# Performance work log

Hardware: AMD Instinct MI355X
Metric: run time of the kernel (lower is better)

Reference implementation:

```python
import jax, jax.numpy as jnp
import numpy as np
import math

INC, OUTC, N, STRIDE = 128, 256, 9, 1
B, H, W = 8, 64, 64
EPS = 1e-5


def setup_inputs() -> dict:
    key = jax.random.key(0)
    k0, k1, k2, k3 = jax.random.split(key, 4)
    x = jax.random.normal(k0, (B, INC, H, W), jnp.float32)
    # p_conv: 3x3 conv inc -> 2N (torch inits weight=0; use small random so offsets are nontrivial)
    pw = jax.random.normal(k1, (2 * N, INC, 3, 3), jnp.float32) * 0.01
    pb = jax.random.normal(k2, (2 * N,), jnp.float32) * 0.01
    # final 1x1 conv inc -> outc (bias=None in the module), BN affine params
    cw = jax.random.normal(k3, (OUTC, INC, 1, 1), jnp.float32) * (1.0 / math.sqrt(INC))
    gamma = jnp.ones((OUTC,), jnp.float32)
    beta = jnp.zeros((OUTC,), jnp.float32)
    return dict(x=x, pw=pw, pb=pb, cw=cw, gamma=gamma, beta=beta)


def _akconv(x, pw, pb, cw, gamma, beta):
    b, c, Hx, Wx = x.shape
    # offset = p_conv(x): 3x3 conv, padding 1, stride STRIDE -> (b, 2N, h, w)
    offset = jax.lax.conv_general_dilated(
        x, pw, window_strides=(STRIDE, STRIDE), padding=((1, 1), (1, 1)),
        dimension_numbers=("NCHW", "OIHW", "NCHW")) + pb[None, :, None, None]
    h, w = offset.shape[2], offset.shape[3]

    # p_n: N points on unit circle (x=cos, y=sin), concat -> (2N,)
    angles = jnp.linspace(0.0, 2.0 * math.pi, N + 1)[:-1]
    p_n = jnp.concatenate([jnp.cos(angles), jnp.sin(angles)])  # (2N,)

    # p_0: base grid positions, (2N, h, w)
    gx = jnp.broadcast_to((jnp.arange(h, dtype=jnp.float32) * STRIDE)[:, None], (h, w))
    gy = jnp.broadcast_to((jnp.arange(w, dtype=jnp.float32) * STRIDE)[None, :], (h, w))
    p0 = jnp.concatenate([jnp.broadcast_to(gx[None], (N, h, w)),
                          jnp.broadcast_to(gy[None], (N, h, w))], axis=0)

    p = (offset + p_n[None, :, None, None] + p0[None]).transpose(0, 2, 3, 1)  # (b,h,w,2N)
    px, py = p[..., :N], p[..., N:]

    fx = jnp.floor(jax.lax.stop_gradient(px))  # q is detached in the original
    fy = jnp.floor(jax.lax.stop_gradient(py))
    q_ltx = jnp.clip(fx, 0, Hx - 1)
    q_lty = jnp.clip(fy, 0, Wx - 1)
    q_rbx = jnp.clip(fx + 1.0, 0, Hx - 1)
    q_rby = jnp.clip(fy + 1.0, 0, Wx - 1)
    pxc = jnp.clip(px, 0, Hx - 1)
    pyc = jnp.clip(py, 0, Wx - 1)

    g_lt = (1.0 + (q_ltx - pxc)) * (1.0 + (q_lty - pyc))
    g_rb = (1.0 - (q_rbx - pxc)) * (1.0 - (q_rby - pyc))
    g_lb = (1.0 + (q_ltx - pxc)) * (1.0 - (q_rby - pyc))
    g_rt = (1.0 - (q_rbx - pxc)) * (1.0 + (q_lty - pyc))

    x_flat = x.reshape(b, c, Hx * Wx)

    def gather(qx, qy):
        idx = (qx * Wx + qy).astype(jnp.int32).reshape(b, -1)  # (b, h*w*N)
        xg = jax.vmap(lambda xf, ix: xf[:, ix])(x_flat, idx)    # (b, c, h*w*N)
        return xg.reshape(b, c, h, w, N)

    x_off = (g_lt[:, None] * gather(q_ltx, q_lty)
             + g_rb[:, None] * gather(q_rbx, q_rby)
             + g_lb[:, None] * gather(q_ltx, q_rby)
             + g_rt[:, None] * gather(q_rbx, q_lty))  # (b,c,h,w,N)

    x_off = x_off.reshape(b, c, h, w * N)  # 'b c h w n -> b c h (w n)'

    # 1x1 conv (no bias) + BatchNorm (training-mode batch stats) + SiLU
    y = jnp.einsum("bchw,oc->bohw", x_off, cw[:, :, 0, 0])
    mean = jnp.mean(y, axis=(0, 2, 3), keepdims=True)
    var = jnp.var(y, axis=(0, 2, 3), keepdims=True)
    yn = (y - mean) * jax.lax.rsqrt(var + EPS)
    yn = yn * gamma[None, :, None, None] + beta[None, :, None, None]
    return yn * jax.nn.sigmoid(yn)


def reference(x, pw, pb, cw, gamma, beta):
    return _akconv(x, pw, pb, cw, gamma, beta)
```

## Files before the change

kernel.cpp:

```cpp
#include <hip/hip_runtime.h>
#include <math.h>

#define INC   128
#define OUTC  256
#define NPTS  9
#define BATCH 8
#define HDIM  64
#define WDIM  64
#define HW    4096
#define JLB   36864
#define JTOT  294912
#define NTOTF 294912.0f

typedef __bf16 bf16x8 __attribute__((ext_vector_type(8)));
typedef float  f32x4  __attribute__((ext_vector_type(4)));

__global__ void k_cvt_cw(const float* __restrict__ cw, __bf16* __restrict__ cwb) {
    int i = blockIdx.x * 256 + threadIdx.x;
    if (i < OUTC * INC) cwb[i] = (__bf16)cw[i];
}

__global__ __launch_bounds__(256) void k_transpose(
        const float* __restrict__ x, __bf16* __restrict__ xTb) {
    __shared__ __bf16 t[64 * 128];
    char* tb = (char*)t;
    int b   = blockIdx.x >> 6;
    int hw0 = (blockIdx.x & 63) << 6;
    int tid = threadIdx.x;
    int lane = tid & 63;
    int cq  = tid >> 6;
    const float* xb = x + b * (INC * HW);
    #pragma unroll
    for (int cc = 0; cc < INC; cc += 4) {
        int c = cc + cq;
        float v = xb[c * HW + hw0 + lane];
        *(__bf16*)(tb + lane * 256 + ((2 * c) ^ ((lane & 15) << 4))) = (__bf16)v;
    }
    __syncthreads();
    __bf16* ob = xTb + ((size_t)b * HW + hw0) * INC;
    #pragma unroll
    for (int i = 0; i < 4; ++i) {
        int chunk = i * 256 + tid;
        int hw  = chunk >> 4;
        int c16 = chunk & 15;
        bf16x8 vv = *(bf16x8*)(tb + hw * 256 + ((c16 * 16) ^ ((hw & 15) << 4)));
        *(bf16x8*)(ob + hw * INC + c16 * 8) = vv;
    }
}

__global__ __launch_bounds__(256) void k_prep(
        const float* __restrict__ x, const float* __restrict__ pw,
        const float* __restrict__ pb, int4* __restrict__ sidx,
        float4* __restrict__ sw) {
    int n  = blockIdx.x >> 7;
    int sp = ((blockIdx.x & 127) << 8) + threadIdx.x;
    int b  = sp >> 12;
    int hh = (sp >> 6) & 63;
    int ww = sp & 63;

    __shared__ float pwl[INC * 9 * 2];
    for (int i = threadIdx.x; i < INC * 9; i += 256) {
        pwl[i * 2 + 0] = pw[n * (INC * 9) + i];
        pwl[i * 2 + 1] = pw[(n + 9) * (INC * 9) + i];
    }
    __syncthreads();

    const float* xb = x + b * (INC * HW);
    float ax = 0.f, ay = 0.f;
    for (int c = 0; c < INC; ++c) {
        const float* xc = xb + c * HW;
        const float* pc = pwl + c * 18;
        #pragma unroll
        for (int ky = 0; ky < 3; ++ky) {
            int yy = hh - 1 + ky;
            #pragma unroll
            for (int kx = 0; kx < 3; ++kx) {
                int xx = ww - 1 + kx;
                float v = ((unsigned)yy < 64u && (unsigned)xx < 64u)
                            ? xc[yy * 64 + xx] : 0.f;
                int k = ky * 3 + kx;
                ax = fmaf(v, pc[k * 2 + 0], ax);
                ay = fmaf(v, pc[k * 2 + 1], ay);
            }
        }
    }
    ax += pb[n];
    ay += pb[n + 9];

    const float TWO_PI = 6.28318530717958647692f;
    float ang = (float)n * (TWO_PI / 9.0f);
    float px = ax + cosf(ang) + (float)hh;
    float py = ay + sinf(ang) + (float)ww;
    float fx = floorf(px), fy = floorf(py);
    float ltx = fminf(fmaxf(fx,        0.f), 63.f);
    float lty = fminf(fmaxf(fy,        0.f), 63.f);
    float rbx = fminf(fmaxf(fx + 1.f,  0.f), 63.f);
    float rby = fminf(fmaxf(fy + 1.f,  0.f), 63.f);
    float pxc = fminf(fmaxf(px,        0.f), 63.f);
    float pyc = fminf(fmaxf(py,        0.f), 63.f);
    float glt = (1.f + ltx - pxc) * (1.f + lty - pyc);
    float grb = (1.f - rbx + pxc) * (1.f - rby + pyc);
    float glb = (1.f + ltx - pxc) * (1.f - rby + pyc);
    float grt = (1.f - rbx + pxc) * (1.f + lty - pyc);

    int j = b * JLB + (hh * 64 + ww) * 9 + n;
    sidx[j] = make_int4((int)ltx * 64 + (int)lty,
                        (int)rbx * 64 + (int)rby,
                        (int)ltx * 64 + (int)rby,
                        (int)rbx * 64 + (int)lty);
    sw[j] = make_float4(glt, grb, glb, grt);
}

template <bool WRITE>
__global__ __launch_bounds__(256, 2) void k_gemm(
        const __bf16* __restrict__ xTb, const __bf16* __restrict__ cwb,
        const int4* __restrict__ sidx, const float4* __restrict__ sw,
        const float* __restrict__ scaleb, const float* __restrict__ shiftb,
        float* __restrict__ gstat, float* __restrict__ out) {
    __shared__ uint4 xoffT4[64 * 256 / 16];
    __shared__ float saux[512];
    char* xoffT = (char*)xoffT4;

    int bidx = blockIdx.x;
    int b    = bidx / 576;
    int jl0  = (bidx % 576) * 64;
    int tid  = threadIdx.x;
    int w    = tid >> 6;
    int l    = tid & 63;

    int col = tid >> 2;
    int q   = tid & 3;
    int j   = b * JLB + jl0 + col;
    int4   qi = sidx[j];
    float4 qw = sw[j];
    const __bf16* xtb = xTb + (size_t)b * (HW * INC) + q * 32;

    float accc[32];
    #pragma unroll
    for (int i = 0; i < 32; ++i) accc[i] = 0.f;

    const int   idx4[4] = { qi.x, qi.y, qi.z, qi.w };
    const float wt4[4]  = { qw.x, qw.y, qw.z, qw.w };
    #pragma unroll
    for (int p = 0; p < 4; ++p) {
        const __bf16* rp = xtb + idx4[p] * INC;
        float wp = wt4[p];
        #pragma unroll
        for (int v = 0; v < 4; ++v) {
            bf16x8 vv = *(const bf16x8*)(rp + v * 8);
            #pragma unroll
            for (int i = 0; i < 8; ++i)
                accc[v * 8 + i] = fmaf(wp, (float)vv[i], accc[v * 8 + i]);
        }
    }
    #pragma unroll
    for (int i8 = 0; i8 < 4; ++i8) {
        bf16x8 pk;
        #pragma unroll
        for (int i = 0; i < 8; ++i) pk[i] = (__bf16)accc[i8 * 8 + i];
        int colbyte = (q * 64 + i8 * 16) ^ ((col & 7) << 4);
        *(bf16x8*)(xoffT + col * 256 + colbyte) = pk;
    }

    if (WRITE) {
        saux[tid]       = scaleb[tid];
        saux[256 + tid] = shiftb[tid];
    }

    if (WRITE) {
        bf16x8 bfrag[4][4];
        #pragma unroll
        for (int ot = 0; ot < 4; ++ot) {
            int o = w * 64 + ot * 16 + (l & 15);
            #pragma unroll
            for (int ks = 0; ks < 4; ++ks) {
                int k = ks * 32 + (l >> 4) * 8;
                bfrag[ot][ks] = *(const bf16x8*)(cwb + o * 128 + k);
            }
        }
        __syncthreads();

        f32x4 acc[4][4] = {};
        #pragma unroll
        for (int ks = 0; ks < 4; ++ks) {
            bf16x8 afrag[4];
            #pragma unroll
            for (int jt = 0; jt < 4; ++jt) {
                int row = jt * 16 + (l & 15);
                int colbyte = (ks * 64 + (l >> 4) * 16) ^ ((row & 7) << 4);
                afrag[jt] = *(const bf16x8*)(xoffT + row * 256 + colbyte);
            }
            #pragma unroll
            for (int jt = 0; jt < 4; ++jt)
                #pragma unroll
                for (int ot = 0; ot < 4; ++ot)
                    acc[jt][ot] = __builtin_amdgcn_mfma_f32_16x16x32_bf16(
                        afrag[jt], bfrag[ot][ks], acc[jt][ot], 0, 0, 0);
        }

        float* outb = out + (size_t)b * (OUTC * JLB);
        #pragma unroll
        for (int ot = 0; ot < 4; ++ot) {
            int o = w * 64 + ot * 16 + (l & 15);
            float sc = saux[o];
            float sh = saux[256 + o];
            float* orow = outb + (size_t)o * JLB + jl0 + (l >> 4) * 4;
            #pragma unroll
            for (int jt = 0; jt < 4; ++jt) {
                f32x4 vst;
                #pragma unroll
                for (int r = 0; r < 4; ++r) {
                    float yn = fmaf(acc[jt][ot][r], sc, sh);
                    vst[r] = yn / (1.f + __expf(-yn));
                }
                *(f32x4*)(orow + jt * 16) = vst;
            }
        }
    } else {
        bf16x8 afrag[4][4];
        #pragma unroll
        for (int mt = 0; mt < 4; ++mt) {
            int m = w * 64 + mt * 16 + (l & 15);
            #pragma unroll
            for (int ks = 0; ks < 4; ++ks) {
                int k = ks * 32 + (l >> 4) * 8;
                afrag[mt][ks] = *(const bf16x8*)(cwb + m * 128 + k);
            }
        }
        __syncthreads();

        f32x4 acc[4][4] = {};
        #pragma unroll
        for (int ks = 0; ks < 4; ++ks) {
            bf16x8 bfrag[4];
            #pragma unroll
            for (int nt = 0; nt < 4; ++nt) {
                int row = nt * 16 + (l & 15);
                int colbyte = (ks * 64 + (l >> 4) * 16) ^ ((row & 7) << 4);
                bfrag[nt] = *(const bf16x8*)(xoffT + row * 256 + colbyte);
            }
            #pragma unroll
            for (int mt = 0; mt < 4; ++mt)
                #pragma unroll
                for (int nt = 0; nt < 4; ++nt)
                    acc[mt][nt] = __builtin_amdgcn_mfma_f32_16x16x32_bf16(
                        afrag[mt][ks], bfrag[nt], acc[mt][nt], 0, 0, 0);
        }

        float* ssum = saux;
        float* ssq  = saux + 256;
        #pragma unroll
        for (int mt = 0; mt < 4; ++mt) {
            #pragma unroll
            for (int r = 0; r < 4; ++r) {
                float s = 0.f, qq = 0.f;
                #pragma unroll
                for (int nt = 0; nt < 4; ++nt) {
                    float v = acc[mt][nt][r];
                    s  += v;
                    qq += v * v;
                }
                #pragma unroll
                for (int d = 1; d < 16; d <<= 1) {
                    s  += __shfl_xor(s, d, 64);
                    qq += __shfl_xor(qq, d, 64);
                }
                if ((l & 15) == 0) {
                    int row = w * 64 + mt * 16 + (l >> 4) * 4 + r;
                    ssum[row] = s;
                    ssq[row]  = qq;
                }
            }
        }
        __syncthreads();
        float* gs = gstat + (bidx & 63) * 512;
        atomicAdd(gs + tid,       ssum[tid]);
        atomicAdd(gs + 256 + tid, ssq[tid]);
    }
}

__global__ void k_stats(const float* __restrict__ gstat,
                        const float* __restrict__ gamma,
                        const float* __restrict__ beta,
                        float* __restrict__ scaleb, float* __restrict__ shiftb) {
    int t = threadIdx.x;
    float s = 0.f, q = 0.f;
    for (int r = 0; r < 64; ++r) {
        s += gstat[r * 512 + t];
        q += gstat[r * 512 + 256 + t];
    }
    float mean = s / NTOTF;
    float var  = q / NTOTF - mean * mean;
    float rstd = rsqrtf(var + 1e-5f);
    float sc = rstd * gamma[t];
    scaleb[t] = sc;
    shiftb[t] = beta[t] - mean * sc;
}

extern "C" void kernel_launch(void* const* d_in, const int* in_sizes, int n_in,
                              void* d_out, int out_size, void* d_ws, size_t ws_size,
                              hipStream_t stream) {
    (void)in_sizes; (void)n_in; (void)out_size; (void)ws_size;
    const float* x     = (const float*)d_in[0];
    const float* pw    = (const float*)d_in[1];
    const float* pb    = (const float*)d_in[2];
    const float* cw    = (const float*)d_in[3];
    const float* gamma = (const float*)d_in[4];
    const float* beta  = (const float*)d_in[5];
    float* out = (float*)d_out;

    char* ws = (char*)d_ws;
    __bf16* xTb   = (__bf16*)(ws);
    int4*   sidx  = (int4*)(ws + 8388608);
    float4* swt   = (float4*)(ws + 13107200);
    __bf16* cwb   = (__bf16*)(ws + 17825792);
    float*  gstat = (float*)(ws + 17891328);
    float*  scaleb= (float*)(ws + 18022400);
    float*  shiftb= (float*)(ws + 18023424);

    hipMemsetAsync(gstat, 0, 64 * 512 * 4, stream);
    k_cvt_cw<<<128, 256, 0, stream>>>(cw, cwb);
    k_transpose<<<512, 256, 0, stream>>>(x, xTb);
    k_prep<<<9 * 128, 256, 0, stream>>>(x, pw, pb, sidx, swt);
    k_gemm<false><<<4608, 256, 0, stream>>>(xTb, cwb, sidx, swt,
                                            nullptr, nullptr, gstat, nullptr);
    k_stats<<<1, 256, 0, stream>>>(gstat, gamma, beta, scaleb, shiftb);
    k_gemm<true><<<4608, 256, 0, stream>>>(xTb, cwb, sidx, swt,
                                           scaleb, shiftb, gstat, out);
}
```

Measured before the change: 227.1 us.

## Store pre-norm GEMM output in bf16 and normalize in a separate pass

Instead of running the gather+GEMM twice (once for batch stats, once to write), the GEMM runs once, writes the unnormalized output as bf16 to workspace, and accumulates stats. A separate elementwise kernel then applies BN scale/shift and SiLU. This removes the redundant gather and MFMA pass but adds a bf16 round-trip of the output (about 150MB write+read) and a rounding step before normalization. It falls back to the old path when the workspace is too small.

```diff
diff --git a/kernel.cpp b/kernel.cpp
--- a/kernel.cpp
+++ b/kernel.cpp
@@ -13,6 +13,7 @@
 #define NTOTF 294912.0f
 
 typedef __bf16 bf16x8 __attribute__((ext_vector_type(8)));
+typedef __bf16 bf16x4 __attribute__((ext_vector_type(4)));
 typedef float  f32x4  __attribute__((ext_vector_type(4)));
 
 __global__ void k_cvt_cw(const float* __restrict__ cw, __bf16* __restrict__ cwb) {
@@ -111,6 +112,163 @@
     sw[j] = make_float4(glt, grb, glb, grt);
 }
 
+__device__ __forceinline__ void gather_tile(
+        const __bf16* __restrict__ xTb, const int4* __restrict__ sidx,
+        const float4* __restrict__ sw, int b, int jl0, int tid, char* xoffT) {
+    int col = tid >> 2;
+    int q   = tid & 3;
+    int j   = b * JLB + jl0 + col;
+    int4   qi = sidx[j];
+    float4 qw = sw[j];
+    const __bf16* xtb = xTb + (size_t)b * (HW * INC) + q * 32;
+
+    float accc[32];
+    #pragma unroll
+    for (int i = 0; i < 32; ++i) accc[i] = 0.f;
+
+    const int   idx4[4] = { qi.x, qi.y, qi.z, qi.w };
+    const float wt4[4]  = { qw.x, qw.y, qw.z, qw.w };
+    #pragma unroll
+    for (int p = 0; p < 4; ++p) {
+        const __bf16* rp = xtb + idx4[p] * INC;
+        float wp = wt4[p];
+        #pragma unroll
+        for (int v = 0; v < 4; ++v) {
+            bf16x8 vv = *(const bf16x8*)(rp + v * 8);
+            #pragma unroll
+            for (int i = 0; i < 8; ++i)
+                accc[v * 8 + i] = fmaf(wp, (float)vv[i], accc[v * 8 + i]);
+        }
+    }
+    #pragma unroll
+    for (int i8 = 0; i8 < 4; ++i8) {
+        bf16x8 pk;
+        #pragma unroll
+        for (int i = 0; i < 8; ++i) pk[i] = (__bf16)accc[i8 * 8 + i];
+        int colbyte = (q * 64 + i8 * 16) ^ ((col & 7) << 4);
+        *(bf16x8*)(xoffT + col * 256 + colbyte) = pk;
+    }
+}
+
+__global__ __launch_bounds__(256, 2) void k_gemm_fused(
+        const __bf16* __restrict__ xTb, const __bf16* __restrict__ cwb,
+        const int4* __restrict__ sidx, const float4* __restrict__ sw,
+        float* __restrict__ gstat, __bf16* __restrict__ yb) {
+    __shared__ uint4 xoffT4[64 * 256 / 16];
+    __shared__ float saux[512];
+    char* xoffT = (char*)xoffT4;
+
+    int bidx = blockIdx.x;
+    int b    = bidx / 576;
+    int jl0  = (bidx % 576) * 64;
+    int tid  = threadIdx.x;
+    int w    = tid >> 6;
+    int l    = tid & 63;
+
+    gather_tile(xTb, sidx, sw, b, jl0, tid, xoffT);
+
+    bf16x8 bfrag[4][4];
+    #pragma unroll
+    for (int ot = 0; ot < 4; ++ot) {
+        int o = w * 64 + ot * 16 + (l & 15);
+        #pragma unroll
+        for (int ks = 0; ks < 4; ++ks) {
+            int k = ks * 32 + (l >> 4) * 8;
+            bfrag[ot][ks] = *(const bf16x8*)(cwb + o * 128 + k);
+        }
+    }
+    __syncthreads();
+
+    f32x4 acc[4][4] = {};
+    #pragma unroll
+    for (int ks = 0; ks < 4; ++ks) {
+        bf16x8 afrag[4];
+        #pragma unroll
+        for (int jt = 0; jt < 4; ++jt) {
+            int row = jt * 16 + (l & 15);
+            int colbyte = (ks * 64 + (l >> 4) * 16) ^ ((row & 7) << 4);
+            afrag[jt] = *(const bf16x8*)(xoffT + row * 256 + colbyte);
+        }
+        #pragma unroll
+        for (int jt = 0; jt < 4; ++jt)
+            #pragma unroll
+            for (int ot = 0; ot < 4; ++ot)
+                acc[jt][ot] = __builtin_amdgcn_mfma_f32_16x16x32_bf16(
+                    afrag[jt], bfrag[ot][ks], acc[jt][ot], 0, 0, 0);
+    }
+
+    __bf16* ybb = yb + (size_t)b * (OUTC * JLB);
+    #pragma unroll
+    for (int ot = 0; ot < 4; ++ot) {
+        int o = w * 64 + ot * 16 + (l & 15);
+        __bf16* yrow = ybb + (size_t)o * JLB + jl0 + (l >> 4) * 4;
+        #pragma unroll
+        for (int jt = 0; jt < 4; ++jt) {
+            bf16x4 pk;
+            #pragma unroll
+            for (int r = 0; r < 4; ++r) pk[r] = (__bf16)acc[jt][ot][r];
+            *(bf16x4*)(yrow + jt * 16) = pk;
+        }
+    }
+
+    float* ssum = saux;
+    float* ssq  = saux + 256;
+    #pragma unroll
+    for (int ot = 0; ot < 4; ++ot) {
+        float s = 0.f, qq = 0.f;
+        #pragma unroll
+        for (int jt = 0; jt < 4; ++jt)
+            #pragma unroll
+            for (int r = 0; r < 4; ++r) {
+                float v = acc[jt][ot][r];
+                s  += v;
+                qq += v * v;
+            }
+        s  += __shfl_xor(s, 16);
+        s  += __shfl_xor(s, 32);
+        qq += __shfl_xor(qq, 16);
+        qq += __shfl_xor(qq, 32);
+        if (l < 16) {
+            int o = w * 64 + ot * 16 + l;
+            ssum[o] = s;
+            ssq[o]  = qq;
+        }
+    }
+    __syncthreads();
+    float* gs = gstat + (bidx & 63) * 512;
+    atomicAdd(gs + tid,       ssum[tid]);
+    atomicAdd(gs + 256 + tid, ssq[tid]);
+}
+
+__global__ __launch_bounds__(256) void k_norm(
+        const __bf16* __restrict__ yb, const float* __restrict__ scaleb,
+        const float* __restrict__ shiftb, float* __restrict__ out) {
+    int base = blockIdx.x * 2048;
+    #pragma unroll
+    for (int it = 0; it < 8; ++it) {
+        int chunk = base + it * 256 + threadIdx.x;
+        int row = (unsigned)chunk / 4608u;
+        int o   = row & 255;
+        float sc = scaleb[o];
+        float sh = shiftb[o];
+        bf16x8 v = *(const bf16x8*)(yb + (size_t)chunk * 8);
+        f32x4 r0, r1;
+        #pragma unroll
+        for (int k = 0; k < 4; ++k) {
+            float yn = fmaf((float)v[k], sc, sh);
+            r0[k] = yn / (1.f + __expf(-yn));
+        }
+        #pragma unroll
+        for (int k = 0; k < 4; ++k) {
+            float yn = fmaf((float)v[4 + k], sc, sh);
+            r1[k] = yn / (1.f + __expf(-yn));
+        }
+        float* op = out + (size_t)chunk * 8;
+        *(f32x4*)op       = r0;
+        *(f32x4*)(op + 4) = r1;
+    }
+}
+
 template <bool WRITE>
 __global__ __launch_bounds__(256, 2) void k_gemm(
         const __bf16* __restrict__ xTb, const __bf16* __restrict__ cwb,
@@ -128,46 +286,11 @@
     int w    = tid >> 6;
     int l    = tid & 63;
 
-    int col = tid >> 2;
-    int q   = tid & 3;
-    int j   = b * JLB + jl0 + col;
-    int4   qi = sidx[j];
-    float4 qw = sw[j];
-    const __bf16* xtb = xTb + (size_t)b * (HW * INC) + q * 32;
-
-    float accc[32];
-    #pragma unroll
-    for (int i = 0; i < 32; ++i) accc[i] = 0.f;
-
-    const int   idx4[4] = { qi.x, qi.y, qi.z, qi.w };
-    const float wt4[4]  = { qw.x, qw.y, qw.z, qw.w };
-    #pragma unroll
-    for (int p = 0; p < 4; ++p) {
-        const __bf16* rp = xtb + idx4[p] * INC;
-        float wp = wt4[p];
-        #pragma unroll
-        for (int v = 0; v < 4; ++v) {
-            bf16x8 vv = *(const bf16x8*)(rp + v * 8);
-            #pragma unroll
-            for (int i = 0; i < 8; ++i)
-                accc[v * 8 + i] = fmaf(wp, (float)vv[i], accc[v * 8 + i]);
-        }
-    }
-    #pragma unroll
-    for (int i8 = 0; i8 < 4; ++i8) {
-        bf16x8 pk;
-        #pragma unroll
-        for (int i = 0; i < 8; ++i) pk[i] = (__bf16)accc[i8 * 8 + i];
-        int colbyte = (q * 64 + i8 * 16) ^ ((col & 7) << 4);
-        *(bf16x8*)(xoffT + col * 256 + colbyte) = pk;
-    }
+    gather_tile(xTb, sidx, sw, b, jl0, tid, xoffT);
 
     if (WRITE) {
         saux[tid]       = scaleb[tid];
         saux[256 + tid] = shiftb[tid];
-    }
-
-    if (WRITE) {
         bf16x8 bfrag[4][4];
         #pragma unroll
         for (int ot = 0; ot < 4; ++ot) {
@@ -300,7 +423,7 @@
 extern "C" void kernel_launch(void* const* d_in, const int* in_sizes, int n_in,
                               void* d_out, int out_size, void* d_ws, size_t ws_size,
                               hipStream_t stream) {
-    (void)in_sizes; (void)n_in; (void)out_size; (void)ws_size;
+    (void)in_sizes; (void)n_in; (void)out_size;
     const float* x     = (const float*)d_in[0];
     const float* pw    = (const float*)d_in[1];
     const float* pb    = (const float*)d_in[2];
@@ -310,21 +433,32 @@
     float* out = (float*)d_out;
 
     char* ws = (char*)d_ws;
-    __bf16* xTb   = (__bf16*)(ws);
-    int4*   sidx  = (int4*)(ws + 8388608);
-    float4* swt   = (float4*)(ws + 13107200);
-    __bf16* cwb   = (__bf16*)(ws + 17825792);
-    float*  gstat = (float*)(ws + 17891328);
-    float*  scaleb= (float*)(ws + 18022400);
-    float*  shiftb= (float*)(ws + 18023424);
+    const size_t Y_BYTES = (size_t)JTOT * OUTC * 2;
+    bool big = ws_size >= (Y_BYTES + 18087936ull);
+
+    size_t off = big ? Y_BYTES : 0;
+    __bf16* yb    = (__bf16*)ws;
+    __bf16* xTb   = (__bf16*)(ws + off);
+    int4*   sidx  = (int4*)(ws + off + 8388608);
+    float4* swt   = (float4*)(ws + off + 13107200);
+    __bf16* cwb   = (__bf16*)(ws + off + 17825792);
+    float*  gstat = (float*)(ws + off + 17891328);
+    float*  scaleb= (float*)(ws + off + 18022400);
+    float*  shiftb= (float*)(ws + off + 18023424);
 
     hipMemsetAsync(gstat, 0, 64 * 512 * 4, stream);
     k_cvt_cw<<<128, 256, 0, stream>>>(cw, cwb);
     k_transpose<<<512, 256, 0, stream>>>(x, xTb);
     k_prep<<<9 * 128, 256, 0, stream>>>(x, pw, pb, sidx, swt);
-    k_gemm<false><<<4608, 256, 0, stream>>>(xTb, cwb, sidx, swt,
-                                            nullptr, nullptr, gstat, nullptr);
-    k_stats<<<1, 256, 0, stream>>>(gstat, gamma, beta, scaleb, shiftb);
-    k_gemm<true><<<4608, 256, 0, stream>>>(xTb, cwb, sidx, swt,
-                                           scaleb, shiftb, gstat, out);
-}
+    if (big) {
+        k_gemm_fused<<<4608, 256, 0, stream>>>(xTb, cwb, sidx, swt, gstat, yb);
+        k_stats<<<1, 256, 0, stream>>>(gstat, gamma, beta, scaleb, shiftb);
+        k_norm<<<4608, 256, 0, stream>>>(yb, scaleb, shiftb, out);
+    } else {
+        k_gemm<false><<<4608, 256, 0, stream>>>(xTb, cwb, sidx, swt,
+                                                nullptr, nullptr, gstat, nullptr);
+        k_stats<<<1, 256, 0, stream>>>(gstat, gamma, beta, scaleb, shiftb);
+        k_gemm<true><<<4608, 256, 0, stream>>>(xTb, cwb, sidx, swt,
+                                               scaleb, shiftb, gstat, out);
+    }
+}
```

Result: slower. 270.5 us (+19.2%).
